# Kernel optimization log

Measured on AMD Instinct MI355X. Metric: run time of the kernel, lower is better.

## Reference

```python
import jax, jax.numpy as jnp
import numpy as np

G, NPG, HC, LAT, FF, EDIM, EH = 8, 4096, 16, 64, 512, 3, 64
N = G * NPG            # 32768 total nodes
E = 393216             # avg degree 12


def setup_inputs() -> dict:
    key = jax.random.key(0)
    ks = jax.random.split(key, 16)
    w = lambda k, s: jax.random.normal(k, s, jnp.float32) * 0.02
    inp = {
        "x": jax.random.normal(ks[0], (G, LAT), jnp.float32),
        "edge_index": jax.random.randint(ks[1], (2, E), 0, N, dtype=jnp.int64),
        "edge_attr": jax.random.normal(ks[2], (E, EDIM), jnp.float32),
        "fc2_w": w(ks[3], (LAT, FF)),   "fc2_b": jnp.zeros((FF,), jnp.float32),
        "fc1_w": w(ks[4], (FF, NPG * HC)), "fc1_b": jnp.zeros((NPG * HC,), jnp.float32),
    }
    for i in range(2):
        inp[f"conv{i}_root"] = w(ks[5 + 4 * i], (HC, HC))
        inp[f"conv{i}_bias"] = jnp.zeros((HC,), jnp.float32)
        inp[f"conv{i}_w1"] = w(ks[6 + 4 * i], (EDIM, EH))
        inp[f"conv{i}_b1"] = jnp.zeros((EH,), jnp.float32)
        inp[f"conv{i}_w2"] = w(ks[7 + 4 * i], (EH, HC * HC))
        inp[f"conv{i}_b2"] = jnp.zeros((HC * HC,), jnp.float32)
    return inp


def _nnconv(x, src, dst, ea, root, bias, w1, b1, w2, b2):
    # edge-conditioned conv (NNConv): per-edge weight matrix from edge MLP
    theta = (jax.nn.relu(ea @ w1 + b1) @ w2 + b2).reshape(-1, HC, HC)  # [E,HC,HC]
    msg = jnp.einsum('ei,eio->eo', x[src], theta)                       # gather+per-edge matvec
    aggr = jax.ops.segment_sum(msg, dst, num_segments=N)                # scatter-add
    return x @ root + aggr + bias


def reference(x, edge_index, edge_attr, fc2_w, fc2_b, fc1_w, fc1_b,
              conv0_root, conv0_bias, conv0_w1, conv0_b1, conv0_w2, conv0_b2,
              conv1_root, conv1_bias, conv1_w1, conv1_b1, conv1_w2, conv1_b2):
    h = x @ fc2_w + fc2_b                      # [G, FF]
    h = jax.nn.elu(h @ fc1_w + fc1_b)          # [G, NPG*HC]
    h = h.reshape(N, HC)                       # node features
    src, dst = edge_index[0], edge_index[1]
    convs = ((conv0_root, conv0_bias, conv0_w1, conv0_b1, conv0_w2, conv0_b2),
             (conv1_root, conv1_bias, conv1_w1, conv1_b1, conv1_w2, conv1_b2))
    for (root, b, w1, b1, w2, b2) in convs:
        h = jax.nn.elu(_nnconv(h, src, dst, edge_attr, root, b, w1, b1, w2, b2))
        # dropout is identity in eval mode
    return h
```

## Files before the change

kernel.cpp:

```cpp
#include <hip/hip_runtime.h>
#include <math.h>

#define G_   8
#define NPG_ 4096
#define HC_  16
#define LAT_ 64
#define FF_  512
#define EDIM_ 3
#define EH_  64
#define NN_  32768
#define EE_  393216

__global__ void k_front1(const float* __restrict__ x, const float* __restrict__ w,
                         const float* __restrict__ b, float* __restrict__ h1) {
  int c = blockIdx.x * blockDim.x + threadIdx.x;
  if (c >= FF_) return;
  float acc[G_];
#pragma unroll
  for (int g = 0; g < G_; g++) acc[g] = 0.f;
  for (int r = 0; r < LAT_; r++) {
    float wv = w[r * FF_ + c];
#pragma unroll
    for (int g = 0; g < G_; g++) acc[g] = fmaf(x[g * LAT_ + r], wv, acc[g]);
  }
#pragma unroll
  for (int g = 0; g < G_; g++) h1[g * FF_ + c] = acc[g] + b[c];
}

__global__ __launch_bounds__(512) void k_front2(const float* __restrict__ h1,
                                                const float* __restrict__ w,
                                                const float* __restrict__ b,
                                                float* __restrict__ hn) {
  __shared__ float sh[G_ * FF_];
  for (int i = threadIdx.x; i < G_ * FF_; i += blockDim.x) sh[i] = h1[i];
  __syncthreads();
  int g = threadIdx.x >> 6;
  int lane = threadIdx.x & 63;
  int c = blockIdx.x * 64 + lane;
  const float* shg = &sh[g * FF_];
  float acc = 0.f;
#pragma unroll 8
  for (int r = 0; r < FF_; r++) acc = fmaf(shg[r], w[r * (NPG_ * HC_) + c], acc);
  float v = acc + b[c];
  hn[g * (NPG_ * HC_) + c] = v > 0.f ? v : expm1f(v);
}

__global__ void k_zero(int* __restrict__ p, int nv) {
  int i = blockIdx.x * blockDim.x + threadIdx.x;
  if (i < nv) p[i] = 0;
}
__global__ void k_hist(const int* __restrict__ key, int* __restrict__ cnt) {
  int e = blockIdx.x * blockDim.x + threadIdx.x;
  if (e < EE_) atomicAdd(&cnt[key[e]], 1);
}
__global__ __launch_bounds__(1024) void k_scan(const int* __restrict__ cnt,
                                               int* __restrict__ rowptr,
                                               int* __restrict__ cursor) {
  __shared__ int part[1024];
  int t = threadIdx.x;
  int base = t * 32;
  int loc[32];
  int s = 0;
#pragma unroll
  for (int i = 0; i < 32; i++) { loc[i] = s; s += cnt[base + i]; }
  part[t] = s;
  __syncthreads();
  for (int off = 1; off < 1024; off <<= 1) {
    int v = (t >= off) ? part[t - off] : 0;
    __syncthreads();
    part[t] += v;
    __syncthreads();
  }
  int pre = (t == 0) ? 0 : part[t - 1];
#pragma unroll
  for (int i = 0; i < 32; i++) {
    int v = pre + loc[i];
    rowptr[base + i] = v;
    cursor[base + i] = v;
  }
  if (t == 1023) rowptr[NN_] = part[1023];
}
__global__ void k_scatter(const int* __restrict__ src, const int* __restrict__ dst,
                          const float* __restrict__ ea, int* __restrict__ cursor,
                          float4* __restrict__ eas4) {
  int e = blockIdx.x * blockDim.x + threadIdx.x;
  if (e < EE_) {
    int pos = atomicAdd(&cursor[src[e]], 1);
    eas4[pos] = make_float4(ea[e * 3], ea[e * 3 + 1], ea[e * 3 + 2],
                            __int_as_float(dst[e]));
  } else if (e < EE_ + 8) {
    eas4[e] = make_float4(0.f, 0.f, 0.f, __int_as_float(0));
  }
}

__global__ void k_wprep(const float* __restrict__ w2, const float* __restrict__ w1,
                        const float* __restrict__ b1, float* __restrict__ W2m,
                        float4* __restrict__ w1p4) {
  int idx = blockIdx.x * 256 + threadIdx.x;
  if (idx < 16384) {
    int i  = idx >> 10;
    int j4 = (idx >> 8) & 3;
    int l  = (idx >> 2) & 63;
    int c  = idx & 3;
    int q = l >> 4, o = l & 15;
    int h = q * 16 + j4 * 4 + c;
    W2m[idx] = w2[h * 256 + i * 16 + o];
  }
  if (idx < 64) {
    w1p4[idx] = make_float4(w1[idx], w1[64 + idx], w1[128 + idx], b1[idx]);
  }
}

__global__ __launch_bounds__(256, 4) void k_node(
    const float* __restrict__ hin, const int do_elu,
    const float* __restrict__ root, const float* __restrict__ bias,
    const float* __restrict__ W2m, float* __restrict__ hnode,
    float* __restrict__ hnext, float4* __restrict__ Mbuf4) {
  __shared__ float sx[256];
  int tid = threadIdx.x;
  int wave = tid >> 6, l = tid & 63;
  int n0 = (blockIdx.x * 4 + wave) * 4;
  float* swx = &sx[wave * 64];

  float v = hin[n0 * 16 + l];
  if (do_elu) {
    v = v > 0.f ? v : expm1f(v);
    hnode[n0 * 16 + l] = v;
  }
  swx[l] = v;

  int nd = l >> 4, o = l & 15;
  float acc = bias[o];
#pragma unroll
  for (int i = 0; i < 16; i++)
    acc = fmaf(swx[nd * 16 + i], root[i * 16 + o], acc);
  hnext[(n0 + nd) * 16 + o] = acc;

  const float4* __restrict__ W2m4 = (const float4*)W2m;
  float4 a0[4], a1[4], a2[4], a3[4];
#pragma unroll
  for (int j4 = 0; j4 < 4; j4++) {
    a0[j4] = make_float4(0.f, 0.f, 0.f, 0.f);
    a1[j4] = make_float4(0.f, 0.f, 0.f, 0.f);
    a2[j4] = make_float4(0.f, 0.f, 0.f, 0.f);
    a3[j4] = make_float4(0.f, 0.f, 0.f, 0.f);
  }
  for (int i = 0; i < 16; i++) {
    float x0 = swx[i];
    float x1 = swx[16 + i];
    float x2 = swx[32 + i];
    float x3 = swx[48 + i];
#pragma unroll
    for (int j4 = 0; j4 < 4; j4++) {
      float4 w = W2m4[i * 256 + j4 * 64 + l];
      a0[j4].x = fmaf(x0, w.x, a0[j4].x); a0[j4].y = fmaf(x0, w.y, a0[j4].y);
      a0[j4].z = fmaf(x0, w.z, a0[j4].z); a0[j4].w = fmaf(x0, w.w, a0[j4].w);
      a1[j4].x = fmaf(x1, w.x, a1[j4].x); a1[j4].y = fmaf(x1, w.y, a1[j4].y);
      a1[j4].z = fmaf(x1, w.z, a1[j4].z); a1[j4].w = fmaf(x1, w.w, a1[j4].w);
      a2[j4].x = fmaf(x2, w.x, a2[j4].x); a2[j4].y = fmaf(x2, w.y, a2[j4].y);
      a2[j4].z = fmaf(x2, w.z, a2[j4].z); a2[j4].w = fmaf(x2, w.w, a2[j4].w);
      a3[j4].x = fmaf(x3, w.x, a3[j4].x); a3[j4].y = fmaf(x3, w.y, a3[j4].y);
      a3[j4].z = fmaf(x3, w.z, a3[j4].z); a3[j4].w = fmaf(x3, w.w, a3[j4].w);
    }
  }
  int s0 = n0 * 256;
#pragma unroll
  for (int j4 = 0; j4 < 4; j4++) Mbuf4[s0 + j4 * 64 + l] = a0[j4];
#pragma unroll
  for (int j4 = 0; j4 < 4; j4++) Mbuf4[s0 + 256 + j4 * 64 + l] = a1[j4];
#pragma unroll
  for (int j4 = 0; j4 < 4; j4++) Mbuf4[s0 + 512 + j4 * 64 + l] = a2[j4];
#pragma unroll
  for (int j4 = 0; j4 < 4; j4++) Mbuf4[s0 + 768 + j4 * 64 + l] = a3[j4];
}

__global__ __launch_bounds__(256, 4) void k_edge(
    const float* __restrict__ hn, const int* __restrict__ rowptr,
    const float4* __restrict__ eas4, const float4* __restrict__ w1p4,
    const float* __restrict__ b2, const float4* __restrict__ Mbuf4,
    float* __restrict__ hnext) {
  __shared__ float4 sw1[4 * 17];
  int tid = threadIdx.x;
  if (tid < 64) sw1[(tid >> 4) * 17 + (tid & 15)] = w1p4[tid];
  __syncthreads();

  int wave = tid >> 6, l = tid & 63;
  int o = l & 15, q = l >> 4;
  int n = blockIdx.x * 4 + wave;

  int rs = rowptr[n], re = rowptr[n + 1];
  if (rs >= re) return;

  int mb = n * 256 + l;
  float4 m0 = Mbuf4[mb], m1 = Mbuf4[mb + 64], m2 = Mbuf4[mb + 128],
         m3 = Mbuf4[mb + 192];
  float M[16] = {m0.x, m0.y, m0.z, m0.w, m1.x, m1.y, m1.z, m1.w,
                 m2.x, m2.y, m2.z, m2.w, m3.x, m3.y, m3.z, m3.w};

  const float4* __restrict__ hx4 = (const float4*)&hn[n * 16];
  float T = 0.f;
#pragma unroll
  for (int i4 = 0; i4 < 4; i4++) {
    float4 xq = hx4[i4];
    T = fmaf(xq.x, b2[(i4 * 4 + 0) * 16 + o], T);
    T = fmaf(xq.y, b2[(i4 * 4 + 1) * 16 + o], T);
    T = fmaf(xq.z, b2[(i4 * 4 + 2) * 16 + o], T);
    T = fmaf(xq.w, b2[(i4 * 4 + 3) * 16 + o], T);
  }

  const float4* __restrict__ w1v = &sw1[q * 17];

  float4 c0 = eas4[rs], c1 = eas4[rs + 1], c2 = eas4[rs + 2], c3 = eas4[rs + 3];
  for (int k = rs; k < re; k += 4) {
    float4 n0 = eas4[k + 4], n1 = eas4[k + 5], n2 = eas4[k + 6], n3 = eas4[k + 7];

    float p0 = 0.f, p1 = 0.f, p2 = 0.f, p3 = 0.f;
#pragma unroll
    for (int j = 0; j < 16; j++) {
      float4 wv = w1v[j];
      float m = M[j];
      float h0 = fmaxf(fmaf(c0.z, wv.z, fmaf(c0.y, wv.y, fmaf(c0.x, wv.x, wv.w))), 0.f);
      float h1 = fmaxf(fmaf(c1.z, wv.z, fmaf(c1.y, wv.y, fmaf(c1.x, wv.x, wv.w))), 0.f);
      float h2 = fmaxf(fmaf(c2.z, wv.z, fmaf(c2.y, wv.y, fmaf(c2.x, wv.x, wv.w))), 0.f);
      float h3 = fmaxf(fmaf(c3.z, wv.z, fmaf(c3.y, wv.y, fmaf(c3.x, wv.x, wv.w))), 0.f);
      p0 = fmaf(h0, m, p0);
      p1 = fmaf(h1, m, p1);
      p2 = fmaf(h2, m, p2);
      p3 = fmaf(h3, m, p3);
    }
    p0 += __shfl_xor(p0, 16); p1 += __shfl_xor(p1, 16);
    p2 += __shfl_xor(p2, 16); p3 += __shfl_xor(p3, 16);
    p0 += __shfl_xor(p0, 32); p1 += __shfl_xor(p1, 32);
    p2 += __shfl_xor(p2, 32); p3 += __shfl_xor(p3, 32);

    float vv  = (q == 0) ? p0   : (q == 1) ? p1   : (q == 2) ? p2   : p3;
    float dpf = (q == 0) ? c0.w : (q == 1) ? c1.w : (q == 2) ? c2.w : c3.w;
    if (k + q < re) atomicAdd(&hnext[__float_as_int(dpf) * 16 + o], vv + T);

    c0 = n0; c1 = n1; c2 = n2; c3 = n3;
  }
}

__global__ void k_elu(const float* __restrict__ in, float* __restrict__ out) {
  int idx = blockIdx.x * blockDim.x + threadIdx.x;
  if (idx >= NN_ * HC_) return;
  float v = in[idx];
  out[idx] = v > 0.f ? v : expm1f(v);
}

extern "C" void kernel_launch(void* const* d_in, const int* in_sizes, int n_in,
                              void* d_out, int out_size, void* d_ws, size_t ws_size,
                              hipStream_t stream) {
  const float* x    = (const float*)d_in[0];
  const int*   ei   = (const int*)d_in[1];
  const float* ea   = (const float*)d_in[2];
  const float* fc2w = (const float*)d_in[3];
  const float* fc2b = (const float*)d_in[4];
  const float* fc1w = (const float*)d_in[5];
  const float* fc1b = (const float*)d_in[6];
  float* out = (float*)d_out;

  float* ws = (float*)d_ws;
  float*  h1     = ws;
  float*  hnode  = h1 + 4096;
  float*  hnext  = hnode + (size_t)NN_ * HC_;
  float*  W2m    = hnext + (size_t)NN_ * HC_;
  float4* w1p4   = (float4*)(W2m + 16384);
  float4* eas4   = (float4*)((float*)w1p4 + 256);
  float4* Mbuf4  = (float4*)((float*)eas4 + (size_t)(EE_ + 8) * 4);
  int*    cnt    = (int*)((float*)Mbuf4 + (size_t)NN_ * 1024);
  int*    rowptr = cnt + NN_;
  int*    cursor = rowptr + NN_ + 1;

  const int* src  = ei;
  const int* dstp = ei + EE_;

  k_front1<<<2, 256, 0, stream>>>(x, fc2w, fc2b, h1);
  k_front2<<<1024, 512, 0, stream>>>(h1, fc1w, fc1b, hnode);

  k_zero<<<(NN_ + 255) / 256, 256, 0, stream>>>(cnt, NN_);
  k_hist<<<(EE_ + 255) / 256, 256, 0, stream>>>(src, cnt);
  k_scan<<<1, 1024, 0, stream>>>(cnt, rowptr, cursor);
  k_scatter<<<(EE_ + 8 + 255) / 256, 256, 0, stream>>>(src, dstp, ea, cursor, eas4);

  for (int cv = 0; cv < 2; cv++) {
    const float* root = (const float*)d_in[7 + cv * 6];
    const float* cb   = (const float*)d_in[8 + cv * 6];
    const float* w1   = (const float*)d_in[9 + cv * 6];
    const float* b1   = (const float*)d_in[10 + cv * 6];
    const float* w2   = (const float*)d_in[11 + cv * 6];
    const float* b2   = (const float*)d_in[12 + cv * 6];
    k_wprep<<<64, 256, 0, stream>>>(w2, w1, b1, W2m, w1p4);
    k_node<<<NN_ / 16, 256, 0, stream>>>(cv == 0 ? hnode : hnext, cv,
                                         root, cb, W2m, hnode, hnext, Mbuf4);
    k_edge<<<NN_ / 4, 256, 0, stream>>>(hnode, rowptr, eas4, w1p4, b2, Mbuf4,
                                        hnext);
  }
  k_elu<<<NN_ * HC_ / 256, 256, 0, stream>>>(hnext, out);
}
```

Measured before the change: 358.8 us.

## Compute edge hidden activations once per edge via LDS, pad CSR rows to 8

The edge kernel used to recompute the 64-wide ReLU hidden layer for each edge in every lane group; that is 16x redundant work per edge. Now each lane computes 8 hidden units for one of 8 edges, stores them in shared memory, and the contraction with the per-node matrix M reads from LDS. CSR rows are padded to multiples of 8 in the scan so each chunk of 8 edges is aligned, with a degree limit masking the pad slots. In exchange it adds LDS traffic, more shuffles per edge, a larger padded edge buffer, and reads of uninitialised padded entries that must be masked.

```diff
diff --git a/kernel.cpp b/kernel.cpp
--- a/kernel.cpp
+++ b/kernel.cpp
@@ -10,6 +10,7 @@
 #define EH_  64
 #define NN_  32768
 #define EE_  393216
+#define EPAD_ (EE_ + NN_ * 8 + 32)
 
 __global__ void k_front1(const float* __restrict__ x, const float* __restrict__ w,
                          const float* __restrict__ b, float* __restrict__ h1) {
@@ -62,7 +63,10 @@
   int loc[32];
   int s = 0;
 #pragma unroll
-  for (int i = 0; i < 32; i++) { loc[i] = s; s += cnt[base + i]; }
+  for (int i = 0; i < 32; i++) {
+    loc[i] = s;
+    s += (cnt[base + i] + 7) & ~7;
+  }
   part[t] = s;
   __syncthreads();
   for (int off = 1; off < 1024; off <<= 1) {
@@ -84,13 +88,10 @@
                           const float* __restrict__ ea, int* __restrict__ cursor,
                           float4* __restrict__ eas4) {
   int e = blockIdx.x * blockDim.x + threadIdx.x;
-  if (e < EE_) {
-    int pos = atomicAdd(&cursor[src[e]], 1);
-    eas4[pos] = make_float4(ea[e * 3], ea[e * 3 + 1], ea[e * 3 + 2],
-                            __int_as_float(dst[e]));
-  } else if (e < EE_ + 8) {
-    eas4[e] = make_float4(0.f, 0.f, 0.f, __int_as_float(0));
-  }
+  if (e >= EE_) return;
+  int pos = atomicAdd(&cursor[src[e]], 1);
+  eas4[pos] = make_float4(ea[e * 3], ea[e * 3 + 1], ea[e * 3 + 2],
+                          __int_as_float(dst[e]));
 }
 
 __global__ void k_wprep(const float* __restrict__ w2, const float* __restrict__ w1,
@@ -176,20 +177,27 @@
 
 __global__ __launch_bounds__(256, 4) void k_edge(
     const float* __restrict__ hn, const int* __restrict__ rowptr,
-    const float4* __restrict__ eas4, const float4* __restrict__ w1p4,
-    const float* __restrict__ b2, const float4* __restrict__ Mbuf4,
-    float* __restrict__ hnext) {
-  __shared__ float4 sw1[4 * 17];
+    const int* __restrict__ cntr, const float4* __restrict__ eas4,
+    const float4* __restrict__ w1p4, const float* __restrict__ b2,
+    const float4* __restrict__ Mbuf4, float* __restrict__ hnext) {
+  __shared__ float4 sw1t[64];
+  __shared__ float shid[4 * 544];
   int tid = threadIdx.x;
-  if (tid < 64) sw1[(tid >> 4) * 17 + (tid & 15)] = w1p4[tid];
+  if (tid < 64) sw1t[(tid & 7) * 8 + (tid >> 3)] = w1p4[tid];
   __syncthreads();
 
   int wave = tid >> 6, l = tid & 63;
   int o = l & 15, q = l >> 4;
+  int es = l & 7, hg = l >> 3;
   int n = blockIdx.x * 4 + wave;
 
-  int rs = rowptr[n], re = rowptr[n + 1];
-  if (rs >= re) return;
+  int deg = cntr[n];
+  if (deg <= 0) return;
+  int rs = rowptr[n];
+  int re = rs + ((deg + 7) & ~7);
+  int limit = rs + deg;
+
+  float* __restrict__ hid = &shid[wave * 544];
 
   int mb = n * 256 + l;
   float4 m0 = Mbuf4[mb], m1 = Mbuf4[mb + 64], m2 = Mbuf4[mb + 128],
@@ -208,36 +216,60 @@
     T = fmaf(xq.w, b2[(i4 * 4 + 3) * 16 + o], T);
   }
 
-  const float4* __restrict__ w1v = &sw1[q * 17];
-
-  float4 c0 = eas4[rs], c1 = eas4[rs + 1], c2 = eas4[rs + 2], c3 = eas4[rs + 3];
-  for (int k = rs; k < re; k += 4) {
-    float4 n0 = eas4[k + 4], n1 = eas4[k + 5], n2 = eas4[k + 6], n3 = eas4[k + 7];
-
-    float p0 = 0.f, p1 = 0.f, p2 = 0.f, p3 = 0.f;
-#pragma unroll
-    for (int j = 0; j < 16; j++) {
-      float4 wv = w1v[j];
-      float m = M[j];
-      float h0 = fmaxf(fmaf(c0.z, wv.z, fmaf(c0.y, wv.y, fmaf(c0.x, wv.x, wv.w))), 0.f);
-      float h1 = fmaxf(fmaf(c1.z, wv.z, fmaf(c1.y, wv.y, fmaf(c1.x, wv.x, wv.w))), 0.f);
-      float h2 = fmaxf(fmaf(c2.z, wv.z, fmaf(c2.y, wv.y, fmaf(c2.x, wv.x, wv.w))), 0.f);
-      float h3 = fmaxf(fmaf(c3.z, wv.z, fmaf(c3.y, wv.y, fmaf(c3.x, wv.x, wv.w))), 0.f);
-      p0 = fmaf(h0, m, p0);
-      p1 = fmaf(h1, m, p1);
-      p2 = fmaf(h2, m, p2);
-      p3 = fmaf(h3, m, p3);
+  float4 cur = eas4[rs + es];
+  for (int k = rs; k < re; k += 8) {
+    float4 nxt = eas4[k + 8 + es];
+
+#pragma unroll
+    for (int jj = 0; jj < 2; jj++) {
+      float4 w0 = sw1t[(jj * 4 + 0) * 8 + hg];
+      float4 w1q = sw1t[(jj * 4 + 1) * 8 + hg];
+      float4 w2q = sw1t[(jj * 4 + 2) * 8 + hg];
+      float4 w3q = sw1t[(jj * 4 + 3) * 8 + hg];
+      float4 hv;
+      hv.x = fmaxf(fmaf(cur.z, w0.z, fmaf(cur.y, w0.y, fmaf(cur.x, w0.x, w0.w))), 0.f);
+      hv.y = fmaxf(fmaf(cur.z, w1q.z, fmaf(cur.y, w1q.y, fmaf(cur.x, w1q.x, w1q.w))), 0.f);
+      hv.z = fmaxf(fmaf(cur.z, w2q.z, fmaf(cur.y, w2q.y, fmaf(cur.x, w2q.x, w2q.w))), 0.f);
+      hv.w = fmaxf(fmaf(cur.z, w3q.z, fmaf(cur.y, w3q.y, fmaf(cur.x, w3q.x, w3q.w))), 0.f);
+      *(float4*)&hid[es * 68 + hg * 8 + jj * 4] = hv;
     }
-    p0 += __shfl_xor(p0, 16); p1 += __shfl_xor(p1, 16);
-    p2 += __shfl_xor(p2, 16); p3 += __shfl_xor(p3, 16);
-    p0 += __shfl_xor(p0, 32); p1 += __shfl_xor(p1, 32);
-    p2 += __shfl_xor(p2, 32); p3 += __shfl_xor(p3, 32);
-
-    float vv  = (q == 0) ? p0   : (q == 1) ? p1   : (q == 2) ? p2   : p3;
-    float dpf = (q == 0) ? c0.w : (q == 1) ? c1.w : (q == 2) ? c2.w : c3.w;
-    if (k + q < re) atomicAdd(&hnext[__float_as_int(dpf) * 16 + o], vv + T);
-
-    c0 = n0; c1 = n1; c2 = n2; c3 = n3;
+
+    float curw = cur.w;
+#pragma unroll
+    for (int e2 = 0; e2 < 8; e2 += 2) {
+      const float4* __restrict__ ha = (const float4*)&hid[e2 * 68 + q * 16];
+      const float4* __restrict__ hb = (const float4*)&hid[(e2 + 1) * 68 + q * 16];
+      float4 a0 = ha[0], a1 = ha[1], a2 = ha[2], a3 = ha[3];
+      float4 b0 = hb[0], b1 = hb[1], b2v = hb[2], b3 = hb[3];
+      float pa = 0.f, pb = 0.f;
+      pa = fmaf(a0.x, M[0], pa);  pa = fmaf(a0.y, M[1], pa);
+      pa = fmaf(a0.z, M[2], pa);  pa = fmaf(a0.w, M[3], pa);
+      pa = fmaf(a1.x, M[4], pa);  pa = fmaf(a1.y, M[5], pa);
+      pa = fmaf(a1.z, M[6], pa);  pa = fmaf(a1.w, M[7], pa);
+      pa = fmaf(a2.x, M[8], pa);  pa = fmaf(a2.y, M[9], pa);
+      pa = fmaf(a2.z, M[10], pa); pa = fmaf(a2.w, M[11], pa);
+      pa = fmaf(a3.x, M[12], pa); pa = fmaf(a3.y, M[13], pa);
+      pa = fmaf(a3.z, M[14], pa); pa = fmaf(a3.w, M[15], pa);
+      pb = fmaf(b0.x, M[0], pb);  pb = fmaf(b0.y, M[1], pb);
+      pb = fmaf(b0.z, M[2], pb);  pb = fmaf(b0.w, M[3], pb);
+      pb = fmaf(b1.x, M[4], pb);  pb = fmaf(b1.y, M[5], pb);
+      pb = fmaf(b1.z, M[6], pb);  pb = fmaf(b1.w, M[7], pb);
+      pb = fmaf(b2v.x, M[8], pb); pb = fmaf(b2v.y, M[9], pb);
+      pb = fmaf(b2v.z, M[10], pb);pb = fmaf(b2v.w, M[11], pb);
+      pb = fmaf(b3.x, M[12], pb); pb = fmaf(b3.y, M[13], pb);
+      pb = fmaf(b3.z, M[14], pb); pb = fmaf(b3.w, M[15], pb);
+      pa += __shfl_xor(pa, 16); pb += __shfl_xor(pb, 16);
+      pa += __shfl_xor(pa, 32); pb += __shfl_xor(pb, 32);
+      float d0 = __shfl(curw, e2);
+      float d1 = __shfl(curw, e2 + 1);
+      if (l < 16) {
+        if (k + e2 < limit)
+          atomicAdd(&hnext[__float_as_int(d0) * 16 + o], pa + T);
+        if (k + e2 + 1 < limit)
+          atomicAdd(&hnext[__float_as_int(d1) * 16 + o], pb + T);
+      }
+    }
+    cur = nxt;
   }
 }
 
@@ -264,10 +296,10 @@
   float*  h1     = ws;
   float*  hnode  = h1 + 4096;
   float*  hnext  = hnode + (size_t)NN_ * HC_;
-  float*  W2m    = hnext + (size_t)NN_ * HC_;
+  float*  W2m    = hnext + (size_t)NN_ * HC_ + 16;
   float4* w1p4   = (float4*)(W2m + 16384);
   float4* eas4   = (float4*)((float*)w1p4 + 256);
-  float4* Mbuf4  = (float4*)((float*)eas4 + (size_t)(EE_ + 8) * 4);
+  float4* Mbuf4  = (float4*)((float*)eas4 + (size_t)(EPAD_ + 32) * 4);
   int*    cnt    = (int*)((float*)Mbuf4 + (size_t)NN_ * 1024);
   int*    rowptr = cnt + NN_;
   int*    cursor = rowptr + NN_ + 1;
@@ -281,7 +313,7 @@
   k_zero<<<(NN_ + 255) / 256, 256, 0, stream>>>(cnt, NN_);
   k_hist<<<(EE_ + 255) / 256, 256, 0, stream>>>(src, cnt);
   k_scan<<<1, 1024, 0, stream>>>(cnt, rowptr, cursor);
-  k_scatter<<<(EE_ + 8 + 255) / 256, 256, 0, stream>>>(src, dstp, ea, cursor, eas4);
+  k_scatter<<<(EE_ + 255) / 256, 256, 0, stream>>>(src, dstp, ea, cursor, eas4);
 
   for (int cv = 0; cv < 2; cv++) {
     const float* root = (const float*)d_in[7 + cv * 6];
@@ -293,8 +325,8 @@
     k_wprep<<<64, 256, 0, stream>>>(w2, w1, b1, W2m, w1p4);
     k_node<<<NN_ / 16, 256, 0, stream>>>(cv == 0 ? hnode : hnext, cv,
                                          root, cb, W2m, hnode, hnext, Mbuf4);
-    k_edge<<<NN_ / 4, 256, 0, stream>>>(hnode, rowptr, eas4, w1p4, b2, Mbuf4,
-                                        hnext);
+    k_edge<<<NN_ / 4, 256, 0, stream>>>(hnode, rowptr, cnt, eas4, w1p4, b2,
+                                        Mbuf4, hnext);
   }
   k_elu<<<NN_ * HC_ / 256, 256, 0, stream>>>(hnext, out);
 }
```

Measured after the change: 312.8 us. 1.15x faster.
